# Kernel tuning notes

Measured on AMD Instinct MI355X. Metric: run time of the kernel, lower is better.

The kernel has to match this reference:

```python
import jax, jax.numpy as jnp
import numpy as np

# ---- static config (mirrors CE defaults) ----
PS = 7        # patch size
WS = 27       # search window (per side)
S0 = 4        # query stride (stride0)
KS = 100      # k_s: top-k kept by search
KA = 100      # k_a: top-k used for aggregation
SCALE = 10.0  # softmax_scale
CI = 16       # inter_channels


def conv2d(x, w, b, pad):
    y = jax.lax.conv_general_dilated(
        x, w, (1, 1), [(pad, pad), (pad, pad)],
        dimension_numbers=("NCHW", "OIHW", "NCHW"))
    return y + b[None, :, None, None]


def all_patches(v):
    """[T,C,H,W] -> [T, H*W, C*PS*PS]; top-left anchored PSxPS patches,
    edge-clamped at the border (dnls-style bounded patch extraction)."""
    t, c, h, w = v.shape
    ii = jnp.clip(jnp.arange(h)[:, None] + jnp.arange(PS)[None, :], 0, h - 1)
    jj = jnp.clip(jnp.arange(w)[:, None] + jnp.arange(PS)[None, :], 0, w - 1)
    p = v[:, :, ii][:, :, :, :, jj]          # [T,C,H,PS,W,PS]
    p = p.transpose(0, 2, 4, 1, 3, 5)        # [T,H,W,C,PS,PS]
    return p.reshape(t, h * w, c * PS * PS)


def setup_inputs():
    key = jax.random.key(0)
    ks = jax.random.split(key, 4)
    vid = jax.random.normal(ks[0], (4, 64, 128, 128), jnp.float32)
    g_w = jax.random.normal(ks[1], (CI, 64, 3, 3), jnp.float32) * 0.05
    g_b = jnp.zeros((CI,), jnp.float32)
    theta_w = jax.random.normal(ks[2], (CI, 64, 1, 1), jnp.float32) * 0.1
    theta_b = jnp.zeros((CI,), jnp.float32)
    return {"vid": vid, "g_w": g_w, "g_b": g_b,
            "theta_w": theta_w, "theta_b": theta_b}


def reference(vid, g_w, g_b, theta_w, theta_b):
    t, c, h, w = vid.shape
    nH, nW = h // S0, w // S0
    Q, N = nH * nW, h * w

    # feature extraction (g -> search features, theta -> aggregation values)
    v1 = conv2d(vid, g_w, g_b, 1)          # [T,CI,H,W]
    v2 = conv2d(vid, theta_w, theta_b, 0)  # [T,CI,H,W]

    # windowed k-NN patch search: query grid (stride0) vs all keys (stride1=1)
    P1 = all_patches(v1)                                    # [T,N,D]
    qis = jnp.arange(nH) * S0
    qjs = jnp.arange(nW) * S0
    qflat = (qis[:, None] * w + qjs[None, :]).reshape(-1)   # [Q]
    Pq = P1[:, qflat]                                       # [T,Q,D]
    scores = jnp.einsum("tqd,tnd->tqn", Pq, P1)             # [T,Q,N]

    off = jnp.arange(WS) - WS // 2
    ci = jnp.clip(qis[:, None] + off, 0, h - 1)             # [nH,WS]
    cj = jnp.clip(qjs[:, None] + off, 0, w - 1)             # [nW,WS]
    cand = (ci[:, None, :, None] * w + cj[None, :, None, :]).reshape(Q, WS * WS)
    dists = jnp.take_along_axis(scores, cand[None], axis=2)  # [T,Q,WS*WS]

    d_k, widx = jax.lax.top_k(dists, KS)                    # [T,Q,KS]
    inds = jnp.take_along_axis(jnp.broadcast_to(cand[None], dists.shape),
                               widx, axis=2)                # flat key positions

    # top-k softmax aggregation weights
    wgt = jax.nn.softmax(d_k[..., :KA] * SCALE, axis=-1)    # [T,Q,KA]
    inds_a = inds[..., :KA]

    # wpsum: weighted sum of value patches gathered at neighbor indices,
    # expressed as sparse-scatter matrix @ dense patch matrix
    A = jnp.zeros((t, Q, N), scores.dtype).at[
        jnp.arange(t)[:, None, None],
        jnp.arange(Q)[None, :, None],
        inds_a].add(wgt)                                    # [T,Q,N]
    P2 = all_patches(v2)                                    # [T,N,D]
    z = jnp.einsum("tqn,tnd->tqd", A, P2)                   # [T,Q,CI*PS*PS]

    # ifold: scatter-add overlapping patches + count normalization
    z = z.reshape(t, Q, CI, PS, PS).transpose(0, 2, 1, 3, 4)
    z = z.reshape(t, CI, Q * PS * PS)
    ri = jnp.clip(qis[:, None] + jnp.arange(PS), 0, h - 1)  # [nH,PS]
    rj = jnp.clip(qjs[:, None] + jnp.arange(PS), 0, w - 1)  # [nW,PS]
    pix = (ri[:, None, :, None] * w + rj[None, :, None, :]).reshape(-1)
    Y = jnp.zeros((t, CI, N), z.dtype).at[:, :, pix].add(z)
    Zc = jnp.zeros((N,), z.dtype).at[pix].add(1.0)
    y = (Y / Zc).reshape(t, CI, h, w)
    return y
```

## Files before the change

kernel.cpp:

```cpp
#include <hip/hip_runtime.h>
#include <hip/hip_bf16.h>

#define T_ 4
#define C_ 64
#define H_ 128
#define W_ 128
#define CI_ 16
#define PS_ 7
#define NC_ 729
#define NCP_ 732
#define S0_ 4
#define KS_ 100
#define NQ_ 1024
#define SCALE_ 10.0f
#define HW_ (H_*W_)
#define RW_ 45
#define LCAP_ 768
#define CB_ 8

typedef float v2f __attribute__((ext_vector_type(2)));
#if __has_builtin(__builtin_elementwise_fma)
#define VFMA(a, b, c) __builtin_elementwise_fma((a), (b), (c))
#else
#define VFMA(a, b, c) ((a) * (b) + (c))
#endif

__device__ __forceinline__ float4 colfix(float4 r, bool loB, bool hiB) {
  float4 o;
  o.x = loB ? 0.f : (hiB ? r.y : r.x);
  o.y = loB ? r.x : (hiB ? r.z : r.y);
  o.z = loB ? r.y : (hiB ? r.w : r.z);
  o.w = loB ? r.z : (hiB ? 0.f : r.w);
  return o;
}

__global__ __launch_bounds__(128, 1) void conv_fused_kernel(
    const float* __restrict__ vid, const float* __restrict__ gw,
    const float* __restrict__ gb, const float* __restrict__ tw,
    const float* __restrict__ tb, float4* __restrict__ v1cs,
    float4* __restrict__ v2cs) {
  __shared__ float wls[C_ * 9 * 4];
  __shared__ float tls[C_ * 4];
  const int tid = threadIdx.x;
  const int g = blockIdx.y, t = blockIdx.z;
  for (int m = tid; m < C_ * 9 * 4; m += 128) {
    int co = m & 3, ck = m >> 2;
    wls[m] = gw[((size_t)(g * 4 + co) * C_) * 9 + ck];
  }
  for (int m = tid; m < C_ * 4; m += 128) {
    int o = m & 3, c = m >> 2;
    tls[m] = tw[(g * 4 + o) * C_ + c];
  }
  __syncthreads();
  const int ti0 = (blockIdx.x >> 3) * 16, tj0 = (blockIdx.x & 7) * 16;
  const int u = tid >> 3, v = tid & 7;
  const int i = ti0 + u, j0 = tj0 + 2 * v;
  const int c0 = j0 - 1;
  const int c0c = min(max(c0, 0), W_ - 4);
  const bool loB = (c0 < 0), hiB = (c0 > W_ - 4);
  const int rm1 = max(i - 1, 0), rp1 = min(i + 1, H_ - 1);
  const float mk0 = (i > 0) ? 1.f : 0.f;
  const float mk2 = (i < H_ - 1) ? 1.f : 0.f;
  const int o0 = rm1 * W_ + c0c, o1 = i * W_ + c0c, o2 = rp1 * W_ + c0c;

  float accA[4], accB[4], acc1A[4], acc1B[4];
#pragma unroll
  for (int co = 0; co < 4; ++co) {
    accA[co] = gb[g * 4 + co]; accB[co] = gb[g * 4 + co];
    acc1A[co] = tb[g * 4 + co]; acc1B[co] = tb[g * 4 + co];
  }

  const float* vb = vid + ((size_t)t * C_) * HW_;
#pragma unroll 1
  for (int cb = 0; cb < C_; cb += CB_) {
    float4 r[CB_][3];
#pragma unroll
    for (int c = 0; c < CB_; ++c) {
      const float* p = vb + (size_t)(cb + c) * HW_;
      r[c][0] = *(const float4*)(p + o0);
      r[c][1] = *(const float4*)(p + o1);
      r[c][2] = *(const float4*)(p + o2);
    }
#pragma unroll
    for (int c = 0; c < CB_; ++c) {
      float4 f0 = colfix(r[c][0], loB, hiB);
      float4 f1 = colfix(r[c][1], loB, hiB);
      float4 f2 = colfix(r[c][2], loB, hiB);
      f0.x *= mk0; f0.y *= mk0; f0.z *= mk0; f0.w *= mk0;
      f2.x *= mk2; f2.y *= mk2; f2.z *= mk2; f2.w *= mk2;
      const float* wc = &wls[(cb + c) * 36];
      const float* tc = &tls[(cb + c) * 4];
      float e0[4] = {f0.x, f0.y, f0.z, f0.w};
      float e1[4] = {f1.x, f1.y, f1.z, f1.w};
      float e2[4] = {f2.x, f2.y, f2.z, f2.w};
#pragma unroll
      for (int co = 0; co < 4; ++co) {
        acc1A[co] = fmaf(tc[co], e1[1], acc1A[co]);
        acc1B[co] = fmaf(tc[co], e1[2], acc1B[co]);
      }
#pragma unroll
      for (int kj = 0; kj < 3; ++kj) {
#pragma unroll
        for (int co = 0; co < 4; ++co) {
          accA[co] = fmaf(wc[(0 * 3 + kj) * 4 + co], e0[kj],     accA[co]);
          accB[co] = fmaf(wc[(0 * 3 + kj) * 4 + co], e0[kj + 1], accB[co]);
          accA[co] = fmaf(wc[(1 * 3 + kj) * 4 + co], e1[kj],     accA[co]);
          accB[co] = fmaf(wc[(1 * 3 + kj) * 4 + co], e1[kj + 1], accB[co]);
          accA[co] = fmaf(wc[(2 * 3 + kj) * 4 + co], e2[kj],     accA[co]);
          accB[co] = fmaf(wc[(2 * 3 + kj) * 4 + co], e2[kj + 1], accB[co]);
        }
      }
    }
  }
  const size_t o = ((size_t)g * T_ + t) * HW_ + i * W_ + j0;
  v1cs[o]     = make_float4(accA[0], accA[1], accA[2], accA[3]);
  v1cs[o + 1] = make_float4(accB[0], accB[1], accB[2], accB[3]);
  v2cs[o]     = make_float4(acc1A[0], acc1A[1], acc1A[2], acc1A[3]);
  v2cs[o + 1] = make_float4(acc1B[0], acc1B[1], acc1B[2], acc1B[3]);
}

__global__ __launch_bounds__(512, 2) void dist_kernel(
    const float4* __restrict__ v1cs, float* __restrict__ distG) {
  __shared__ float4 Rs[2][2048];
  const int tid = threadIdx.x;
  const int t = blockIdx.y;
  const int qi0 = (blockIdx.x >> 3) * 16, qj0 = (blockIdx.x & 7) * 16;
  const int w = tid >> 6, lane = tid & 63;
  const int pr = w >> 2, dj = (w & 3) * 4;
  const int rbase = 8 * pr;
  const int qi_p = qi0 + rbase;
  const int qj = qj0 + dj;
  const int la = lane >> 1, bg = lane & 1;
  const int b_lo = max(13 - qj, 0);
  const int bs = bg ? 13 : b_lo;
  const int a_lo0 = max(13 - qi_p, 0);
  const int a_lo1 = max(9 - qi_p, 0);
  const bool compute_ok = (la < 31);

  int soff[4];
#pragma unroll
  for (int k = 0; k < 4; ++k) {
    int p = min(tid + 512 * k, RW_ * RW_ - 1);
    int uu = p / RW_, vv = p - uu * RW_;
    int row = min(max(qi0 - 13 + uu, 0), H_ - 1);
    int col = min(max(qj0 - 13 + vv, 0), W_ - 1);
    soff[k] = row * W_ + col;
  }

  v2f acc0[14], acc1[14];
#pragma unroll
  for (int j = 0; j < 14; ++j) { acc0[j] = (v2f){0.f, 0.f}; acc1[j] = (v2f){0.f, 0.f}; }

  float4 st[4];
  {
    const float4* src = v1cs + ((size_t)0 * T_ + t) * HW_;
#pragma unroll
    for (int k = 0; k < 4; ++k) st[k] = src[soff[k]];
  }
  int cur = 0;
#pragma unroll 1
  for (int cc = 0; cc < 4; ++cc) {
    float4* buf = &Rs[cur][0];
#pragma unroll
    for (int k = 0; k < 4; ++k) buf[tid + 512 * k] = st[k];
    if (cc < 3) {
      const float4* src = v1cs + ((size_t)(cc + 1) * T_ + t) * HW_;
#pragma unroll
      for (int k = 0; k < 4; ++k) st[k] = src[soff[k]];
    }
    __syncthreads();
    if (compute_ok) {
#pragma unroll 1
      for (int r = 0; r < 7; ++r) {
        v2f q0lo[7], q0hi[7], q1lo[7], q1hi[7];
        const float4* q0row = &buf[(rbase + 13 + r) * RW_ + dj + 13];
#pragma unroll
        for (int s = 0; s < 7; ++s) {
          float4 qq = q0row[s];
          q0lo[s] = (v2f){qq.x, qq.y};
          q0hi[s] = (v2f){qq.z, qq.w};
          float4 q2 = q0row[4 * RW_ + s];
          q1lo[s] = (v2f){q2.x, q2.y};
          q1hi[s] = (v2f){q2.z, q2.w};
        }
        const float4* crow = &buf[(rbase + la + r) * RW_ + dj + bs];
#pragma unroll
        for (int y = 0; y < 20; ++y) {
          float4 vv4 = crow[y];
          v2f vlo = (v2f){vv4.x, vv4.y}, vhi = (v2f){vv4.z, vv4.w};
          const int s_lo = (y > 13) ? (y - 13) : 0;
          const int s_hi = (y < 6) ? y : 6;
#pragma unroll
          for (int s = s_lo; s <= s_hi; ++s) {
            int j = y - s;
            acc0[j] = VFMA(q0lo[s], vlo, acc0[j]);
            acc0[j] = VFMA(q0hi[s], vhi, acc0[j]);
            acc1[j] = VFMA(q1lo[s], vlo, acc1[j]);
            acc1[j] = VFMA(q1hi[s], vhi, acc1[j]);
          }
        }
      }
    }
    cur ^= 1;
  }
  if (compute_ok) {
    const int q0q = ((qi_p >> 2) << 5) + (qj >> 2);
    if (la >= a_lo0 && la <= 26) {
      float* out = distG + ((size_t)t * NQ_ + q0q) * NCP_ + la * 27 + bs;
#pragma unroll
      for (int j = 0; j < 14; ++j) out[j] = acc0[j].x + acc0[j].y;
    }
    const int a1 = la - 4;
    if (a1 >= a_lo1 && a1 <= 26) {
      float* out = distG + ((size_t)t * NQ_ + (q0q + 32)) * NCP_ + a1 * 27 + bs;
#pragma unroll
      for (int j = 0; j < 14; ++j) out[j] = acc1[j].x + acc1[j].y;
    }
  }
}

__global__ __launch_bounds__(256) void select_kernel(
    const float* __restrict__ distG, int* __restrict__ sel_n,
    float* __restrict__ sel_w, float* __restrict__ wsum_out) {
  __shared__ float dist[NC_];
  __shared__ unsigned int ukey[NC_];
  __shared__ float redf[4];
  __shared__ unsigned int hist[256];
  __shared__ int lk[LCAP_];
  __shared__ unsigned int lkey[LCAP_];
  __shared__ unsigned int scal[6];

  const int tid = threadIdx.x;
  const int lane = tid & 63, wid = tid >> 6;
  const int q = blockIdx.x, t = blockIdx.y;
  const int qi = (q >> 5) * S0_, qj = (q & 31) * S0_;
  const int a_lo = max(13 - qi, 0), b_lo = max(13 - qj, 0);
  const size_t base = ((size_t)t * NQ_ + q) * NCP_;

  for (int h = tid; h < 256; h += 256) hist[h] = 0;
  if (tid == 0) { scal[2] = 0; scal[3] = 0; }
  float lmax = -INFINITY;
  if (a_lo == 0 && b_lo == 0) {
    if (tid < 182) {
      float4 d4 = *(const float4*)(distG + base + 4 * tid);
      float dv[4] = {d4.x, d4.y, d4.z, d4.w};
#pragma unroll
      for (int e = 0; e < 4; ++e) {
        int k = 4 * tid + e;
        float d = dv[e];
        dist[k] = d;
        unsigned int u = __float_as_uint(d);
        ukey[k] = u ^ (((unsigned int)((int)u >> 31)) | 0x80000000u);
        lmax = fmaxf(lmax, d);
      }
    } else if (tid == 182) {
      float d = distG[base + 728];
      dist[728] = d;
      unsigned int u = __float_as_uint(d);
      ukey[728] = u ^ (((unsigned int)((int)u >> 31)) | 0x80000000u);
      lmax = d;
    }
  } else {
    for (int k = tid; k < NC_; k += 256) {
      int aa = k / 27, bb = k - aa * 27;
      int kk = max(aa, a_lo) * 27 + max(bb, b_lo);
      float d = distG[base + kk];
      dist[k] = d;
      unsigned int u = __float_as_uint(d);
      ukey[k] = u ^ (((unsigned int)((int)u >> 31)) | 0x80000000u);
      lmax = fmaxf(lmax, d);
    }
  }
#pragma unroll
  for (int off = 32; off > 0; off >>= 1)
    lmax = fmaxf(lmax, __shfl_down(lmax, off, 64));
  if (lane == 0) redf[wid] = lmax;
  __syncthreads();
  const float dmax = fmaxf(fmaxf(redf[0], redf[1]), fmaxf(redf[2], redf[3]));
  for (int k = tid; k < NC_; k += 256) atomicAdd(&hist[ukey[k] >> 24], 1u);
  __syncthreads();
  if (wid == 0) {
    int s4 = (int)(hist[lane * 4] + hist[lane * 4 + 1] + hist[lane * 4 + 2] + hist[lane * 4 + 3]);
    int s = s4;
#pragma unroll
    for (int off = 1; off < 64; off <<= 1) {
      int o = __shfl_down(s, off, 64);
      if (lane + off < 64) s += o;
    }
    int above = s - s4;
    if (above < KS_ && s >= KS_) {
      int run = above;
#pragma unroll
      for (int bb = 3; bb >= 0; --bb) {
        int h = (int)hist[lane * 4 + bb];
        if (run + h >= KS_) { scal[0] = (unsigned int)(lane * 4 + bb); scal[1] = (unsigned int)run; break; }
        run += h;
      }
    }
  }
  __syncthreads();
  const unsigned int beta = scal[0];
  const int run = (int)scal[1];
  for (int h = tid; h < 256; h += 256) hist[h] = 0;
  __syncthreads();
  for (int k = tid; k < NC_; k += 256)
    if ((ukey[k] >> 24) == beta) atomicAdd(&hist[(ukey[k] >> 16) & 0xFFu], 1u);
  __syncthreads();
  if (wid == 0) {
    int s4 = (int)(hist[lane * 4] + hist[lane * 4 + 1] + hist[lane * 4 + 2] + hist[lane * 4 + 3]);
    int s = s4;
#pragma unroll
    for (int off = 1; off < 64; off <<= 1) {
      int o = __shfl_down(s, off, 64);
      if (lane + off < 64) s += o;
    }
    int above = run + s - s4;
    if (above < KS_ && run + s >= KS_) {
      int r2 = above;
#pragma unroll
      for (int bb = 3; bb >= 0; --bb) {
        int h = (int)hist[lane * 4 + bb];
        if (r2 + h >= KS_) { scal[4] = (unsigned int)(lane * 4 + bb); scal[5] = (unsigned int)r2; break; }
        r2 += h;
      }
    }
  }
  __syncthreads();
  const unsigned int beta2 = scal[4];
  const int run2 = (int)scal[5];
  const size_t outb = ((size_t)t * NQ_ + q) * KS_;
  float lsum = 0.f;
  for (int k = tid; k < NC_; k += 256) {
    unsigned int key = ukey[k];
    unsigned int bin = key >> 24;
    bool sel = false, bdry = false;
    if (bin > beta) sel = true;
    else if (bin == beta) {
      unsigned int b2 = (key >> 16) & 0xFFu;
      if (b2 > beta2) sel = true;
      else if (b2 == beta2) bdry = true;
    }
    if (sel) {
      unsigned int slot = atomicAdd(&scal[2], 1u);
      int aa = k / 27, bb = k - aa * 27;
      int ni = min(max(qi + aa - 13, 0), H_ - 1);
      int nj = min(max(qj + bb - 13, 0), W_ - 1);
      float wv = __expf(SCALE_ * (dist[k] - dmax));
      sel_n[outb + slot] = (ni << 7) | nj;
      sel_w[outb + slot] = wv;
      lsum += wv;
    } else if (bdry) {
      unsigned int pos = atomicAdd(&scal[3], 1u);
      if (pos < LCAP_) { lk[pos] = k; lkey[pos] = key; }
    }
  }
  __syncthreads();
  const int L = min((int)scal[3], LCAP_);
  for (int i = tid; i < L; i += 256) {
    unsigned int key = lkey[i];
    int k = lk[i];
    int cnt = run2;
    for (int m = 0; m < L; ++m)
      cnt += (int)((lkey[m] > key) || (lkey[m] == key && lk[m] < k));
    if (cnt < KS_) {
      unsigned int slot = atomicAdd(&scal[2], 1u);
      int aa = k / 27, bb = k - aa * 27;
      int ni = min(max(qi + aa - 13, 0), H_ - 1);
      int nj = min(max(qj + bb - 13, 0), W_ - 1);
      float wv = __expf(SCALE_ * (dist[k] - dmax));
      sel_n[outb + slot] = (ni << 7) | nj;
      sel_w[outb + slot] = wv;
      lsum += wv;
    }
  }
#pragma unroll
  for (int off = 32; off > 0; off >>= 1) lsum += __shfl_down(lsum, off, 64);
  __syncthreads();
  if (lane == 0) redf[wid] = lsum;
  __syncthreads();
  if (tid == 0) wsum_out[t * NQ_ + q] = (redf[0] + redf[1]) + (redf[2] + redf[3]);
}

__device__ __forceinline__ int cov_axis(int x) {
  int c = 0;
#pragma unroll
  for (int r = 0; r < 7; ++r) {
    if (x < H_ - 1) {
      int qb = x - r;
      c += (qb >= 0 && (qb & 3) == 0) ? 1 : 0;
    } else {
      c += (r >= 3) ? 1 : 0;
    }
  }
  return c;
}

__global__ __launch_bounds__(1024) void agg_kernel(
    const float4* __restrict__ v2cs, const int* __restrict__ sel_n,
    const float* __restrict__ sel_w, const float* __restrict__ wsum,
    float* __restrict__ Y) {
  __shared__ float4 Rs[RW_ * RW_];
  __shared__ int s_off[16][KS_];
  __shared__ float s_w[16][KS_];
  const int tid = threadIdx.x;
  const int t = blockIdx.y;
  const int qi0 = (blockIdx.x >> 3) * 16, qj0 = (blockIdx.x & 7) * 16;
  const int w = tid >> 6, lane = tid & 63;
  const int di = (w >> 2) * 4, dj = (w & 3) * 4;
  const int qi = qi0 + di, qj = qj0 + dj;
  const int q = ((qi >> 2) << 5) + (qj >> 2);
  const size_t base = ((size_t)t * NQ_ + q) * KS_;
  const float inv = 1.0f / wsum[t * NQ_ + q];
  for (int k = lane; k < KS_; k += 64) {
    int n = sel_n[base + k];
    int ni = n >> 7, nj = n & 127;
    s_off[w][k] = (ni - qi0 + 13) * RW_ + (nj - qj0 + 13);
    s_w[w][k] = sel_w[base + k] * inv;
  }
  const int r = lane / 7, s = lane - r * 7;
  const int myo = r * RW_ + s;
  const int oi = min(qi + r, H_ - 1), oj = min(qj + s, W_ - 1);
  const float invZ = 1.0f / (float)(cov_axis(oi) * cov_axis(oj));
#pragma unroll 1
  for (int cc = 0; cc < 4; ++cc) {
    __syncthreads();
    const float4* src = v2cs + ((size_t)cc * T_ + t) * HW_;
    for (int p = tid; p < RW_ * RW_; p += 1024) {
      int uu = p / RW_, vv = p - uu * RW_;
      int row = min(max(qi0 - 13 + uu, 0), H_ - 1);
      int col = min(max(qj0 - 13 + vv, 0), W_ - 1);
      Rs[p] = src[row * W_ + col];
    }
    __syncthreads();
    if (lane < 49) {
      float4 acc = make_float4(0.f, 0.f, 0.f, 0.f);
#pragma unroll 4
      for (int k = 0; k < KS_; ++k) {
        float wv = s_w[w][k];
        float4 v = Rs[s_off[w][k] + myo];
        acc.x = fmaf(wv, v.x, acc.x);
        acc.y = fmaf(wv, v.y, acc.y);
        acc.z = fmaf(wv, v.z, acc.z);
        acc.w = fmaf(wv, v.w, acc.w);
      }
      float* yb = Y + (((size_t)t * CI_ + cc * 4) * H_ + oi) * W_ + oj;
      atomicAdd(yb, acc.x * invZ);
      atomicAdd(yb + HW_, acc.y * invZ);
      atomicAdd(yb + 2 * HW_, acc.z * invZ);
      atomicAdd(yb + 3 * HW_, acc.w * invZ);
    }
  }
}

extern "C" void kernel_launch(void* const* d_in, const int* in_sizes, int n_in,
                              void* d_out, int out_size, void* d_ws, size_t ws_size,
                              hipStream_t stream) {
  const float* vid     = (const float*)d_in[0];
  const float* g_w     = (const float*)d_in[1];
  const float* g_b     = (const float*)d_in[2];
  const float* theta_w = (const float*)d_in[3];
  const float* theta_b = (const float*)d_in[4];
  float* Y = (float*)d_out;

  float* v1cs  = (float*)d_ws;
  float* v2cs  = v1cs + (size_t)4 * T_ * HW_ * 4;
  float* distG = v2cs + (size_t)4 * T_ * HW_ * 4;
  int*   sel_n = (int*)(distG + (size_t)T_ * NQ_ * NCP_);
  float* sel_w = (float*)(sel_n + (size_t)T_ * NQ_ * KS_);
  float* wsumv = sel_w + (size_t)T_ * NQ_ * KS_;

  hipMemsetAsync(Y, 0, (size_t)out_size * sizeof(float), stream);

  conv_fused_kernel<<<dim3(64, 4, T_), 128, 0, stream>>>(
      vid, g_w, g_b, theta_w, theta_b, (float4*)v1cs, (float4*)v2cs);
  dist_kernel<<<dim3(64, T_), 512, 0, stream>>>((const float4*)v1cs, distG);
  select_kernel<<<dim3(NQ_, T_), 256, 0, stream>>>(distG, sel_n, sel_w, wsumv);
  agg_kernel<<<dim3(64, T_), 1024, 0, stream>>>((const float4*)v2cs, sel_n, sel_w, wsumv, Y);
}
```

Measured before the change: 256.8 us.

## Split distance computation over channel groups into two partial-sum launches

The distance kernel gains a channel base and count, and the host runs it twice over two halves of the channel groups, writing partial distances to two buffers. The selection kernel then sums the two partials while loading. The two launches are issued back to back on the same stream, so they run one after the other with half the loop each, and not concurrently. The split doubles the distance write and read traffic, and it only applies when the workspace is large enough.

```diff
diff --git a/kernel.cpp b/kernel.cpp
--- a/kernel.cpp
+++ b/kernel.cpp
@@ -120,7 +120,8 @@
 }
 
 __global__ __launch_bounds__(512, 2) void dist_kernel(
-    const float4* __restrict__ v1cs, float* __restrict__ distG) {
+    const float4* __restrict__ v1cs, float* __restrict__ out,
+    int cbase, int nch) {
   __shared__ float4 Rs[2][2048];
   const int tid = threadIdx.x;
   const int t = blockIdx.y;
@@ -153,18 +154,18 @@
 
   float4 st[4];
   {
-    const float4* src = v1cs + ((size_t)0 * T_ + t) * HW_;
+    const float4* src = v1cs + ((size_t)cbase * T_ + t) * HW_;
 #pragma unroll
     for (int k = 0; k < 4; ++k) st[k] = src[soff[k]];
   }
   int cur = 0;
 #pragma unroll 1
-  for (int cc = 0; cc < 4; ++cc) {
+  for (int ci = 0; ci < nch; ++ci) {
     float4* buf = &Rs[cur][0];
 #pragma unroll
     for (int k = 0; k < 4; ++k) buf[tid + 512 * k] = st[k];
-    if (cc < 3) {
-      const float4* src = v1cs + ((size_t)(cc + 1) * T_ + t) * HW_;
+    if (ci + 1 < nch) {
+      const float4* src = v1cs + ((size_t)(cbase + ci + 1) * T_ + t) * HW_;
 #pragma unroll
       for (int k = 0; k < 4; ++k) st[k] = src[soff[k]];
     }
@@ -206,22 +207,23 @@
   if (compute_ok) {
     const int q0q = ((qi_p >> 2) << 5) + (qj >> 2);
     if (la >= a_lo0 && la <= 26) {
-      float* out = distG + ((size_t)t * NQ_ + q0q) * NCP_ + la * 27 + bs;
-#pragma unroll
-      for (int j = 0; j < 14; ++j) out[j] = acc0[j].x + acc0[j].y;
+      float* o = out + ((size_t)t * NQ_ + q0q) * NCP_ + la * 27 + bs;
+#pragma unroll
+      for (int j = 0; j < 14; ++j) o[j] = acc0[j].x + acc0[j].y;
     }
     const int a1 = la - 4;
     if (a1 >= a_lo1 && a1 <= 26) {
-      float* out = distG + ((size_t)t * NQ_ + (q0q + 32)) * NCP_ + a1 * 27 + bs;
-#pragma unroll
-      for (int j = 0; j < 14; ++j) out[j] = acc1[j].x + acc1[j].y;
+      float* o = out + ((size_t)t * NQ_ + (q0q + 32)) * NCP_ + a1 * 27 + bs;
+#pragma unroll
+      for (int j = 0; j < 14; ++j) o[j] = acc1[j].x + acc1[j].y;
     }
   }
 }
 
 __global__ __launch_bounds__(256) void select_kernel(
-    const float* __restrict__ distG, int* __restrict__ sel_n,
-    float* __restrict__ sel_w, float* __restrict__ wsum_out) {
+    const float* __restrict__ distA, const float* __restrict__ distB, int dual,
+    int* __restrict__ sel_n, float* __restrict__ sel_w,
+    float* __restrict__ wsum_out) {
   __shared__ float dist[NC_];
   __shared__ unsigned int ukey[NC_];
   __shared__ float redf[4];
@@ -242,7 +244,11 @@
   float lmax = -INFINITY;
   if (a_lo == 0 && b_lo == 0) {
     if (tid < 182) {
-      float4 d4 = *(const float4*)(distG + base + 4 * tid);
+      float4 d4 = *(const float4*)(distA + base + 4 * tid);
+      if (dual) {
+        float4 b4 = *(const float4*)(distB + base + 4 * tid);
+        d4.x += b4.x; d4.y += b4.y; d4.z += b4.z; d4.w += b4.w;
+      }
       float dv[4] = {d4.x, d4.y, d4.z, d4.w};
 #pragma unroll
       for (int e = 0; e < 4; ++e) {
@@ -254,7 +260,8 @@
         lmax = fmaxf(lmax, d);
       }
     } else if (tid == 182) {
-      float d = distG[base + 728];
+      float d = distA[base + 728];
+      if (dual) d += distB[base + 728];
       dist[728] = d;
       unsigned int u = __float_as_uint(d);
       ukey[728] = u ^ (((unsigned int)((int)u >> 31)) | 0x80000000u);
@@ -264,7 +271,8 @@
     for (int k = tid; k < NC_; k += 256) {
       int aa = k / 27, bb = k - aa * 27;
       int kk = max(aa, a_lo) * 27 + max(bb, b_lo);
-      float d = distG[base + kk];
+      float d = distA[base + kk];
+      if (dual) d += distB[base + kk];
       dist[k] = d;
       unsigned int u = __float_as_uint(d);
       ukey[k] = u ^ (((unsigned int)((int)u >> 31)) | 0x80000000u);
@@ -468,12 +476,23 @@
   int*   sel_n = (int*)(distG + (size_t)T_ * NQ_ * NCP_);
   float* sel_w = (float*)(sel_n + (size_t)T_ * NQ_ * KS_);
   float* wsumv = sel_w + (size_t)T_ * NQ_ * KS_;
+  float* distB = wsumv + (size_t)T_ * NQ_;
+
+  const size_t need_dual =
+      ((size_t)4 * T_ * HW_ * 4 * 2 + (size_t)T_ * NQ_ * NCP_ * 2 +
+       (size_t)T_ * NQ_ * KS_ * 2 + (size_t)T_ * NQ_) * sizeof(float);
+  const int dual = (ws_size >= need_dual) ? 1 : 0;
 
   hipMemsetAsync(Y, 0, (size_t)out_size * sizeof(float), stream);
 
   conv_fused_kernel<<<dim3(64, 4, T_), 128, 0, stream>>>(
       vid, g_w, g_b, theta_w, theta_b, (float4*)v1cs, (float4*)v2cs);
-  dist_kernel<<<dim3(64, T_), 512, 0, stream>>>((const float4*)v1cs, distG);
-  select_kernel<<<dim3(NQ_, T_), 256, 0, stream>>>(distG, sel_n, sel_w, wsumv);
+  if (dual) {
+    dist_kernel<<<dim3(64, T_), 512, 0, stream>>>((const float4*)v1cs, distG, 0, 2);
+    dist_kernel<<<dim3(64, T_), 512, 0, stream>>>((const float4*)v1cs, distB, 2, 2);
+  } else {
+    dist_kernel<<<dim3(64, T_), 512, 0, stream>>>((const float4*)v1cs, distG, 0, 4);
+  }
+  select_kernel<<<dim3(NQ_, T_), 256, 0, stream>>>(distG, distB, dual, sel_n, sel_w, wsumv);
   agg_kernel<<<dim3(64, T_), 1024, 0, stream>>>((const float4*)v2cs, sel_n, sel_w, wsumv, Y);
 }
```

Result: slower. 265.4 us (+3.4%).
